# Kernel tuning notes

Hardware: AMD Instinct MI355X
Metric: run time of the kernel (lower is better)

Reference implementation:

```python
import jax, jax.numpy as jnp
import numpy as np
import math
from itertools import combinations

SEQ_LEN = 12
IN_DIM = 1152
D_MODEL = 1152
HEADS = 2
DEPTH = D_MODEL // HEADS
TSS = 3            # temporal_set_size
WAY = 5
SHOT = 5
N_SUPPORT = WAY * SHOT
N_QUERIES = 50
PE_SCALE = 0.1
LN_EPS = 1e-5

# static frame-tuple index table: all C(seq_len, 3) combinations, [T, 3]
TUPLES = np.array(list(combinations(range(SEQ_LEN), TSS)), dtype=np.int32)
T = TUPLES.shape[0]  # 220

def _pe_table():
    pos = np.arange(SEQ_LEN, dtype=np.float64)[:, None]
    div = np.exp(np.arange(0, IN_DIM, 2, dtype=np.float64) * -(math.log(10000.0) / IN_DIM))
    pe = np.zeros((SEQ_LEN, IN_DIM), np.float32)
    pe[:, 0::2] = (np.sin(pos * div) * PE_SCALE).astype(np.float32)
    pe[:, 1::2] = (np.cos(pos * div) * PE_SCALE).astype(np.float32)
    return jnp.asarray(pe)

PE = _pe_table()  # [seq_len, in_dim]

def setup_inputs() -> dict:
    key = jax.random.key(0)
    k0, k1, k2, k3 = jax.random.split(key, 4)
    support_set = jax.random.normal(k0, (N_SUPPORT, SEQ_LEN, IN_DIM), jnp.float32)
    queries = jax.random.normal(k1, (N_QUERIES, SEQ_LEN, IN_DIM), jnp.float32)
    # sorted labels: class c owns support rows [c*SHOT, (c+1)*SHOT)
    support_labels = jnp.repeat(jnp.arange(WAY, dtype=jnp.int32), SHOT)
    k_w = jax.random.normal(k2, (IN_DIM * TSS, D_MODEL), jnp.float32) * 0.02
    k_b = jnp.zeros((D_MODEL,), jnp.float32)
    v_w = jax.random.normal(k3, (IN_DIM * TSS, D_MODEL), jnp.float32) * 0.02
    v_b = jnp.zeros((D_MODEL,), jnp.float32)
    ln_g = jnp.ones((D_MODEL,), jnp.float32)
    ln_b = jnp.zeros((D_MODEL,), jnp.float32)
    return dict(support_set=support_set, queries=queries, support_labels=support_labels,
                k_w=k_w, k_b=k_b, v_w=v_w, v_b=v_b, ln_g=ln_g, ln_b=ln_b)

def _layernorm(x, g, b):
    mu = x.mean(-1, keepdims=True)
    var = ((x - mu) ** 2).mean(-1, keepdims=True)
    return (x - mu) * jax.lax.rsqrt(var + LN_EPS) * g + b

def reference(support_set, queries, support_labels, k_w, k_b, v_w, v_b, ln_g, ln_b):
    nq = queries.shape[0]
    # positional encoding (dropout p=0 -> identity)
    s = support_set + PE
    q = queries + PE
    # temporal tuple gather: [n, T, 3, in_dim] -> [n, T, 3*in_dim]
    s_t = s[:, TUPLES, :].reshape(N_SUPPORT, T, TSS * IN_DIM)
    q_t = q[:, TUPLES, :].reshape(nq, T, TSS * IN_DIM)
    s_ks = _layernorm(s_t @ k_w + k_b, ln_g, ln_b)
    q_ks = _layernorm(q_t @ k_w + k_b, ln_g, ln_b)
    s_vs = s_t @ v_w + v_b
    q_vs = q_t @ v_w + v_b
    # split heads; labels are sorted so class grouping == reshape(way, shot, ...)
    qh = q_ks.reshape(nq, T, HEADS, DEPTH).transpose(0, 2, 1, 3)               # [q,H,T,dh]
    kh = s_ks.reshape(WAY, SHOT, T, HEADS, DEPTH).transpose(0, 1, 3, 2, 4)     # [w,s,H,T,dh]
    vh = s_vs.reshape(WAY, SHOT, T, HEADS, DEPTH).transpose(0, 1, 3, 2, 4)     # [w,s,H,T,dh]
    scores = jnp.einsum('qhtd,wshkd->qwhtsk', qh, kh) / jnp.sqrt(jnp.float32(DEPTH))
    # softmax jointly over (shot, key-tuple) per (query, class, head, query-tuple)
    attn = jax.nn.softmax(scores.reshape(nq, WAY, HEADS, T, SHOT * T), axis=-1)
    attn = attn.reshape(nq, WAY, HEADS, T, SHOT, T)
    # attention output summed over support shots; heads re-concatenated -> prototype
    proto = jnp.einsum('qwhtsk,wshkd->qwthd', attn, vh).reshape(nq, WAY, T, D_MODEL)
    diff = q_vs[:, None, :, :] - proto                                          # [q,w,T,d]
    logits = -(jnp.sum(diff * diff, axis=(-2, -1)) / T)                         # [q,w]
    return logits
```

## Files before the change

### kernel.cpp

```cpp
#include <hip/hip_runtime.h>
#include <math.h>


#define DIM 1152
#define HDIM 576
#define NTUP 220

typedef __attribute__((ext_vector_type(4))) float f32x4;
typedef __attribute__((ext_vector_type(8))) short short8;

__device__ __forceinline__ ushort f2bf(float x) {
  union { float f; unsigned u; } v; v.f = x;
  unsigned r = (v.u + 0x7FFFu + ((v.u >> 16) & 1u)) >> 16;
  return (ushort)r;
}
__device__ __forceinline__ float bf2f(ushort x) {
  union { unsigned u; float f; } v; v.u = ((unsigned)x) << 16;
  return v.f;
}

__global__ __launch_bounds__(256) void init_tables(
    const float* __restrict__ g, const float* __restrict__ bb,
    int* __restrict__ tup, uint* __restrict__ tupP, float* __restrict__ consts)
{
  const int tid = threadIdx.x;
  if (tid < 220) {
    int t = tid, idx = 0;
    for (int a = 0; a < 10; a++)
      for (int b2 = a + 1; b2 < 11; b2++)
        for (int c = b2 + 1; c < 12; c++) {
          if (idx == t) {
            tup[t*3+0]=a; tup[t*3+1]=b2; tup[t*3+2]=c;
            tupP[t] = (uint)a | ((uint)b2 << 8) | ((uint)c << 16);
          }
          idx++;
        }
  }
  __shared__ float rd[6];
  if (tid < 6) rd[tid] = 0.f;
  __syncthreads();
  float s[6] = {0,0,0,0,0,0};
  for (int d = tid; d < DIM; d += 256) {
    float gv = g[d], bv = bb[d];
    int h = (d >= HDIM);
    s[h]     += gv*gv;
    s[2 + h] += gv*bv;
    s[4 + h] += bv*bv;
  }
  for (int i = 0; i < 6; i++) atomicAdd(&rd[i], s[i]);
  __syncthreads();
  if (tid < 6) consts[tid] = rd[tid];
}

__global__ __launch_bounds__(256) void pe_kernel(float* __restrict__ PE)
{
  int idx = blockIdx.x * 256 + threadIdx.x;
  if (idx >= 12 * DIM) return;
  int p = idx / DIM, d = idx - p * DIM;
  int j = d >> 1;
  double div = exp((double)(2 * j) * (-9.210340371976184 / 1152.0));
  double ang = (double)p * div;
  double v = (d & 1) ? cos(ang) : sin(ang);
  PE[idx] = (float)(v * 0.1);
}

__global__ __launch_bounds__(256) void add_pe_bf(
    const float* __restrict__ sup, const float* __restrict__ qry,
    const float* __restrict__ PE, ushort* __restrict__ Fb)
{
  int idx = blockIdx.x * 256 + threadIdx.x;
  if (idx >= 900 * DIM) return;
  int row = idx / DIM, d = idx - row * DIM;
  int p = row % 12;
  float x = (row < 300) ? sup[idx] : qry[idx - 300 * DIM];
  Fb[idx] = f2bf(x + PE[p * DIM + d]);
}

__global__ __launch_bounds__(256) void conv_w(
    const float* __restrict__ kw, const float* __restrict__ vw,
    ushort* __restrict__ Wt)
{
  __shared__ float tileS[32][33];
  const int tid = threadIdx.x;
  const int kt = blockIdx.x * 32;
  const int ng0 = blockIdx.y * 32;
  const int b = ng0 / DIM, d0 = ng0 - b * DIM;
  const float* src = (b < 3) ? (kw + (size_t)b * DIM * DIM)
                             : (vw + (size_t)(b - 3) * DIM * DIM);
  const int r = tid >> 3, cs = (tid & 7) * 4;
  float4 vsrc = *(const float4*)(src + (size_t)(kt + r) * DIM + d0 + cs);
  tileS[r][cs+0] = vsrc.x; tileS[r][cs+1] = vsrc.y;
  tileS[r][cs+2] = vsrc.z; tileS[r][cs+3] = vsrc.w;
  __syncthreads();
  uint u0 = (uint)f2bf(tileS[cs+0][r]) | ((uint)f2bf(tileS[cs+1][r]) << 16);
  uint u1 = (uint)f2bf(tileS[cs+2][r]) | ((uint)f2bf(tileS[cs+3][r]) << 16);
  uint2 o; o.x = u0; o.y = u1;
  *(uint2*)(Wt + (size_t)(ng0 + r) * DIM + kt + cs) = o;
}

__global__ __launch_bounds__(256) void gemm_proj_mfma(
    const ushort* __restrict__ Fb, const ushort* __restrict__ Wt,
    const float* __restrict__ kb, const float* __restrict__ vb,
    float* __restrict__ Ck, float* __restrict__ Cv)
{
  __shared__ __align__(16) ushort As[128][72];
  __shared__ __align__(16) ushort Bs[128][72];
  const int tid = threadIdx.x;
  const int col0 = blockIdx.x * 128;
  const int row0 = blockIdx.y * 128;
  f32x4 acc[4][4] = {};
  const int wv = tid >> 6, lane = tid & 63;
  const int wm = wv >> 1, wn = wv & 1;
  for (int k0 = 0; k0 < DIM; k0 += 64) {
    __syncthreads();
    for (int sidx = tid; sidx < 1024; sidx += 256) {
      int rowa = sidx >> 3, kseg = sidx & 7;
      uint4 va = {0,0,0,0};
      int gm = row0 + rowa;
      if (gm < 900) va = *(const uint4*)(Fb + (size_t)gm * DIM + k0 + kseg * 8);
      *(uint4*)&As[rowa][kseg * 8] = va;
      int gc = col0 + rowa;
      uint4 vb4 = *(const uint4*)(Wt + (size_t)gc * DIM + k0 + kseg * 8);
      *(uint4*)&Bs[rowa][kseg * 8] = vb4;
    }
    __syncthreads();
    #pragma unroll
    for (int ks = 0; ks < 64; ks += 32) {
      short8 a[4], b[4];
      #pragma unroll
      for (int i = 0; i < 4; i++) {
        a[i] = *(const short8*)&As[wm*64 + i*16 + (lane & 15)][ks + (lane >> 4) * 8];
        b[i] = *(const short8*)&Bs[wn*64 + i*16 + (lane & 15)][ks + (lane >> 4) * 8];
      }
      #pragma unroll
      for (int mi = 0; mi < 4; mi++)
        #pragma unroll
        for (int ni = 0; ni < 4; ni++)
          acc[mi][ni] = __builtin_amdgcn_mfma_f32_16x16x32_bf16(a[mi], b[ni], acc[mi][ni], 0, 0, 0);
    }
  }
  const int b = col0 / DIM, d_base = col0 - b * DIM;
  #pragma unroll
  for (int mi = 0; mi < 4; mi++)
    #pragma unroll
    for (int ni = 0; ni < 4; ni++)
      #pragma unroll
      for (int r = 0; r < 4; r++) {
        int m = row0 + wm * 64 + mi * 16 + (lane >> 4) * 4 + r;
        if (m >= 900) continue;
        int n = wn * 64 + ni * 16 + (lane & 15);
        int d = d_base + n;
        float val = acc[mi][ni][r];
        if (b < 3) Ck[((size_t)m * 3 + b)       * DIM + d] = val + kb[d] * (1.f/3.f);
        else       Cv[((size_t)m * 3 + (b - 3)) * DIM + d] = val + vb[d] * (1.f/3.f);
      }
}

__global__ __launch_bounds__(128) void row_stats(
    const float* __restrict__ Ck, const float* __restrict__ g,
    const float* __restrict__ bb, float* __restrict__ m_o,
    float* __restrict__ A_o, float* __restrict__ B_o)
{
  const int r = blockIdx.x, tid = threadIdx.x;
  const float* x = Ck + (size_t)r * DIM;
  float sm = 0, sa0 = 0, sa1 = 0, sb0 = 0, sb1 = 0;
  for (int d = tid; d < DIM; d += 128) {
    float xv = x[d], gv = g[d], bv = bb[d];
    float xg2 = xv * gv * gv, xgb = xv * gv * bv;
    if (d < HDIM) { sa0 += xg2; sb0 += xgb; } else { sa1 += xg2; sb1 += xgb; }
    sm += xv;
  }
  for (int o = 32; o > 0; o >>= 1) {
    sm  += __shfl_down(sm, o);  sa0 += __shfl_down(sa0, o); sa1 += __shfl_down(sa1, o);
    sb0 += __shfl_down(sb0, o); sb1 += __shfl_down(sb1, o);
  }
  __shared__ float red[2][5];
  if ((tid & 63) == 0) {
    int wv = tid >> 6;
    red[wv][0]=sm; red[wv][1]=sa0; red[wv][2]=sa1; red[wv][3]=sb0; red[wv][4]=sb1;
  }
  __syncthreads();
  if (tid == 0) {
    m_o[r]         = (red[0][0] + red[1][0]) * (1.f / 1152.f);
    A_o[r]         =  red[0][1] + red[1][1];
    A_o[2700 + r]  =  red[0][2] + red[1][2];
    B_o[r]         =  red[0][3] + red[1][3];
    B_o[2700 + r]  =  red[0][4] + red[1][4];
  }
}

__global__ __launch_bounds__(256) void self_gram(
    const float* __restrict__ Ck, float* __restrict__ S)
{
  const int u = blockIdx.x, tid = threadIdx.x;
  __shared__ float CS[36][129];
  float acc[2][3] = {{0,0,0},{0,0,0}};
  const int ta = tid / 12, tb = tid - (tid / 12) * 12;
  for (int k0 = 0; k0 < DIM; k0 += 128) {
    __syncthreads();
    for (int idx = tid; idx < 36 * 128; idx += 256) {
      int rr = idx >> 7, kk = idx & 127;
      CS[rr][kk] = Ck[((size_t)u * 36 + rr) * DIM + k0 + kk];
    }
    __syncthreads();
    if (ta < 18) {
      for (int kk = 0; kk < 128; kk++) {
        float va0 = CS[ta*2][kk], va1 = CS[ta*2+1][kk];
        float vb0 = CS[tb*3][kk], vb1 = CS[tb*3+1][kk], vb2 = CS[tb*3+2][kk];
        acc[0][0]+=va0*vb0; acc[0][1]+=va0*vb1; acc[0][2]+=va0*vb2;
        acc[1][0]+=va1*vb0; acc[1][1]+=va1*vb1; acc[1][2]+=va1*vb2;
      }
    }
  }
  if (ta < 18) {
    #pragma unroll
    for (int i = 0; i < 2; i++)
      #pragma unroll
      for (int j = 0; j < 3; j++)
        S[u * 1296 + (ta*2+i) * 36 + tb*3+j] = acc[i][j];
  }
}

__global__ __launch_bounds__(256) void row_ln(
    const float* __restrict__ S, const float* __restrict__ m_i,
    const float* __restrict__ A_i, const float* __restrict__ B_i,
    const int* __restrict__ tup, float4* __restrict__ kst)
{
  const int u = blockIdx.x, tid = threadIdx.x;
  __shared__ float Ss[36][36];
  __shared__ float ms[36], As[2][36], Bs[2][36];
  for (int idx = tid; idx < 1296; idx += 256) (&Ss[0][0])[idx] = S[u * 1296 + idx];
  if (tid < 36) {
    ms[tid]    = m_i[u * 36 + tid];
    As[0][tid] = A_i[u * 36 + tid];  As[1][tid] = A_i[2700 + u * 36 + tid];
    Bs[0][tid] = B_i[u * 36 + tid];  Bs[1][tid] = B_i[2700 + u * 36 + tid];
  }
  __syncthreads();
  if (tid < NTUP) {
    int a0 = tup[tid*3+0]*3+0, a1 = tup[tid*3+1]*3+1, a2 = tup[tid*3+2]*3+2;
    float mu = ms[a0] + ms[a1] + ms[a2];
    float qq = Ss[a0][a0] + Ss[a1][a1] + Ss[a2][a2]
             + 2.f * (Ss[a0][a1] + Ss[a0][a2] + Ss[a1][a2]);
    float var = qq * (1.f / 1152.f) - mu * mu;
    float rr = rsqrtf(var + 1e-5f);
    kst[((size_t)0 * 75 + u) * 220 + tid] =
        make_float4(mu, rr, As[0][a0]+As[0][a1]+As[0][a2], Bs[0][a0]+Bs[0][a1]+Bs[0][a2]);
    kst[((size_t)1 * 75 + u) * 220 + tid] =
        make_float4(mu, rr, As[1][a0]+As[1][a1]+As[1][a2], Bs[1][a0]+Bs[1][a1]+Bs[1][a2]);
  }
}

__global__ __launch_bounds__(256) void conv_ckw(
    const float* __restrict__ Ck, const float* __restrict__ g,
    ushort* __restrict__ Ckw)
{
  size_t i = (size_t)blockIdx.x * 256 + threadIdx.x;
  if (i >= (size_t)2700 * DIM) return;
  int d = (int)(i % DIM);
  Ckw[i] = f2bf(Ck[i] * g[d]);
}

__global__ __launch_bounds__(256) void cross_gram_mfma(
    const ushort* __restrict__ Ckw, ushort* __restrict__ Gb)
{
  __shared__ __align__(16) ushort As[128][72];
  __shared__ __align__(16) ushort Bs[128][72];
  const int tid = threadIdx.x;
  const int col0 = blockIdx.x * 128;
  const int row0 = blockIdx.y * 128;
  const int h = blockIdx.z;
  f32x4 acc[4][4] = {};
  const int wv = tid >> 6, lane = tid & 63;
  const int wm = wv >> 1, wn = wv & 1;
  for (int k0 = 0; k0 < HDIM; k0 += 64) {
    __syncthreads();
    for (int sidx = tid; sidx < 1024; sidx += 256) {
      int rowa = sidx >> 3, kseg = sidx & 7;
      uint4 va = {0,0,0,0};
      int gm = row0 + rowa;
      if (gm < 1800)
        va = *(const uint4*)(Ckw + (size_t)(900 + gm) * DIM + h * HDIM + k0 + kseg * 8);
      *(uint4*)&As[rowa][kseg * 8] = va;
      uint4 vb = {0,0,0,0};
      int gn = col0 + rowa;
      if (gn < 900)
        vb = *(const uint4*)(Ckw + (size_t)gn * DIM + h * HDIM + k0 + kseg * 8);
      *(uint4*)&Bs[rowa][kseg * 8] = vb;
    }
    __syncthreads();
    #pragma unroll
    for (int ks = 0; ks < 64; ks += 32) {
      short8 a[4], b[4];
      #pragma unroll
      for (int i = 0; i < 4; i++) {
        a[i] = *(const short8*)&As[wm*64 + i*16 + (lane & 15)][ks + (lane >> 4) * 8];
        b[i] = *(const short8*)&Bs[wn*64 + i*16 + (lane & 15)][ks + (lane >> 4) * 8];
      }
      #pragma unroll
      for (int mi = 0; mi < 4; mi++)
        #pragma unroll
        for (int ni = 0; ni < 4; ni++)
          acc[mi][ni] = __builtin_amdgcn_mfma_f32_16x16x32_bf16(a[mi], b[ni], acc[mi][ni], 0, 0, 0);
    }
  }
  #pragma unroll
  for (int mi = 0; mi < 4; mi++)
    #pragma unroll
    for (int ni = 0; ni < 4; ni++)
      #pragma unroll
      for (int r = 0; r < 4; r++) {
        int m = row0 + wm * 64 + mi * 16 + (lane >> 4) * 4 + r;
        int n = col0 + wn * 64 + ni * 16 + (lane & 15);
        if (m < 1800 && n < 900)
          Gb[((size_t)h * 1800 + m) * 900 + n] = f2bf(acc[mi][ni][r]);
      }
}

__global__ __launch_bounds__(256) void vt_build(
    const float* __restrict__ Cv, ushort* __restrict__ Vt)
{
  __shared__ ushort T[192][72];
  const int tid = threadIdx.x;
  const int nb = blockIdx.x, z = blockIdx.y;
  const int w = z >> 1, h = z & 1;
  const int n0 = nb * 64;
  for (int idx = tid; idx < 12288; idx += 256) {
    int bin = idx >> 6, nc = idx & 63;
    ushort v = 0;
    if (bin < 180) {
      int s = bin / 36, rem = bin - s * 36, j = rem / 12, p = rem - j * 12;
      v = f2bf(Cv[(size_t)((w*5+s)*36 + p*3 + j) * DIM + h * HDIM + n0 + nc]);
    }
    T[bin][nc] = v;
  }
  __syncthreads();
  for (int u4i = tid; u4i < 1536; u4i += 256) {
    int n = u4i / 24, kc = (u4i - n * 24) * 8;
    ushort tmp[8];
    #pragma unroll
    for (int e = 0; e < 8; e++) tmp[e] = T[kc + e][n];
    *(uint4*)(Vt + ((size_t)z * 576 + n0 + n) * 192 + kc) = *(uint4*)tmp;
  }
}

__global__ __launch_bounds__(256) void attn2(
    const ushort* __restrict__ Gb, const float4* __restrict__ kst,
    const uint* __restrict__ tupP, const float* __restrict__ consts,
    ushort* __restrict__ Mg)
{
  __shared__ __align__(16) ushort GsS[5][36][36];
  __shared__ __align__(16) float4 kstS[5][224];
  __shared__ __align__(16) union UU { ushort Qg[5][16][64]; ushort Ps[2][16][224]; } U;
  __shared__ __align__(16) float4 qstS[112];
  __shared__ uint tupT[224];
  __shared__ float red[4][16];

  const int tid = threadIdx.x;
  const int half = blockIdx.x, w = blockIdx.y;
  const int qu = blockIdx.z >> 1, h = blockIdx.z & 1;
  const float Ggh = consts[h], Gbh = consts[2 + h], Bbh = consts[4 + h];
  const int wv = tid >> 6, lane = tid & 63;
  const int rowg = lane >> 4, col16 = lane & 15;

  for (int idx = tid; idx < 224; idx += 256) tupT[idx] = (idx < 220) ? tupP[idx] : 0u;
  for (int idx = tid; idx < 3240; idx += 256) {
    int s = idx / 648, rem = idx - s * 648, a = rem / 18, bp = rem - a * 18;
    ((uint*)&GsS[s][a][0])[bp] =
      *(const uint*)(Gb + (size_t)(h*1800 + qu*36 + a) * 900 + (w*5+s)*36 + bp*2);
  }
  for (int idx = tid; idx < 1120; idx += 256) {
    int s = idx / 224, k = idx - s * 224;
    float4 v;
    if (k < 220) {
      float4 t4 = kst[((size_t)h*75 + w*5 + s) * 220 + k];
      v = make_float4(t4.x, t4.y, t4.z, (t4.y*(t4.w - t4.x*Gbh) + Bbh) * (1.f/24.f));
    } else v = make_float4(0.f, 0.f, 0.f, -1e30f);
    kstS[s][k] = v;
  }
  for (int idx = tid; idx < 112; idx += 256) {
    int t = half * 112 + idx;
    float4 v = make_float4(0.f, 0.f, 0.f, 0.f);
    if (t < 220) {
      float4 q4 = kst[((size_t)h*75 + 25 + qu) * 220 + t];
      v = make_float4(q4.x, q4.y * (1.f/24.f), q4.z,
                      q4.y * (q4.w - q4.x*Gbh) * (1.f/24.f));
    }
    qstS[idx] = v;
  }
  __syncthreads();

  short8 ebf[4][2];
  #pragma unroll
  for (int i = 0; i < 4; i++) {
    int ntile = wv + 4*i;
    uint tk = tupT[ntile*16 + col16];
    int b0 = (int)(tk & 255u)*3, b1 = (int)((tk>>8)&255u)*3+1, b2 = (int)((tk>>16)&255u)*3+2;
    #pragma unroll
    for (int ks = 0; ks < 2; ks++)
      #pragma unroll
      for (int e = 0; e < 8; e++) {
        int colb = ks*32 + rowg*8 + e;
        ebf[i][ks][e] = (short)((colb==b0 || colb==b1 || colb==b2) ? 0x3F80 : 0);
      }
  }
  short8 lbf[7];
  {
    int bin = wv*16 + col16;
    int j = bin / 12, p = bin - j*12;
    #pragma unroll
    for (int ks = 0; ks < 7; ks++)
      #pragma unroll
      for (int e = 0; e < 8; e++) {
        int k = ks*32 + rowg*8 + e;
        uint tk = tupT[k];
        int f = (j==0) ? (int)(tk & 255u) : (j==1) ? (int)((tk>>8) & 255u)
              : (j==2) ? (int)((tk>>16) & 255u) : 255;
        lbf[ks][e] = (short)((f == p) ? 0x3F80 : 0);
      }
  }

  for (int c = 0; c < 7; c++) {
    const int tbase = (half*7 + c) * 16;
    __syncthreads();
    for (int idx = tid; idx < 5120; idx += 256) {
      int s = idx >> 10, q = (idx >> 6) & 15, b = idx & 63;
      ushort val = 0;
      if (b < 36) {
        uint tq = tupT[tbase + q];
        int a0 = (int)(tq&255u)*3, a1 = (int)((tq>>8)&255u)*3+1, a2 = (int)((tq>>16)&255u)*3+2;
        val = f2bf(bf2f(GsS[s][a0][b]) + bf2f(GsS[s][a1][b]) + bf2f(GsS[s][a2][b]));
      }
      U.Qg[s][q][b] = val;
    }
    __syncthreads();

    float4 q4r[4];
    #pragma unroll
    for (int r = 0; r < 4; r++) q4r[r] = qstS[c*16 + rowg*4 + r];

    f32x4 acc[5][4];
    #pragma unroll
    for (int s = 0; s < 5; s++) {
      short8 af0 = *(const short8*)&U.Qg[s][col16][rowg*8];
      short8 af1 = *(const short8*)&U.Qg[s][col16][32 + rowg*8];
      #pragma unroll
      for (int i = 0; i < 4; i++) {
        int ntile = wv + 4*i;
        if (ntile < 14) {
          f32x4 a4 = {0.f,0.f,0.f,0.f};
          a4 = __builtin_amdgcn_mfma_f32_16x16x32_bf16(af0, ebf[i][0], a4, 0, 0, 0);
          a4 = __builtin_amdgcn_mfma_f32_16x16x32_bf16(af1, ebf[i][1], a4, 0, 0, 0);
          float4 k4 = kstS[s][ntile*16 + col16];
          #pragma unroll
          for (int r = 0; r < 4; r++) {
            float X = a4[r] - k4.x * q4r[r].z - q4r[r].x * (k4.z - k4.x * Ggh);
            a4[r] = q4r[r].y * k4.y * X + q4r[r].w + k4.w;
          }
          acc[s][i] = a4;
        }
      }
    }

    float mxr[4] = {-1e30f,-1e30f,-1e30f,-1e30f};
    #pragma unroll
    for (int s = 0; s < 5; s++)
      #pragma unroll
      for (int i = 0; i < 4; i++)
        if (wv + 4*i < 14) {
          #pragma unroll
          for (int r = 0; r < 4; r++) mxr[r] = fmaxf(mxr[r], acc[s][i][r]);
        }
    #pragma unroll
    for (int o = 8; o > 0; o >>= 1) {
      #pragma unroll
      for (int r = 0; r < 4; r++) mxr[r] = fmaxf(mxr[r], __shfl_xor(mxr[r], o));
    }
    if (col16 == 0) {
      #pragma unroll
      for (int r = 0; r < 4; r++) red[wv][rowg*4 + r] = mxr[r];
    }
    __syncthreads();
    float mxg[4];
    #pragma unroll
    for (int r = 0; r < 4; r++) {
      int row = rowg*4 + r;
      mxg[r] = fmaxf(fmaxf(red[0][row], red[1][row]), fmaxf(red[2][row], red[3][row]));
    }
    __syncthreads();
    float smr[4] = {0.f,0.f,0.f,0.f};
    #pragma unroll
    for (int s = 0; s < 5; s++)
      #pragma unroll
      for (int i = 0; i < 4; i++)
        if (wv + 4*i < 14) {
          #pragma unroll
          for (int r = 0; r < 4; r++) {
            float p = __expf(acc[s][i][r] - mxg[r]);
            acc[s][i][r] = p;
            smr[r] += p;
          }
        }
    #pragma unroll
    for (int o = 8; o > 0; o >>= 1) {
      #pragma unroll
      for (int r = 0; r < 4; r++) smr[r] += __shfl_xor(smr[r], o);
    }
    if (col16 == 0) {
      #pragma unroll
      for (int r = 0; r < 4; r++) red[wv][rowg*4 + r] = smr[r];
    }
    __syncthreads();
    float inv[4];
    #pragma unroll
    for (int r = 0; r < 4; r++) {
      int row = rowg*4 + r;
      inv[r] = 1.0f / (red[0][row] + red[1][row] + red[2][row] + red[3][row]);
    }

    #pragma unroll
    for (int s = 0; s < 5; s++) {
      #pragma unroll
      for (int i = 0; i < 4; i++) {
        int ntile = wv + 4*i;
        if (ntile < 14) {
          #pragma unroll
          for (int r = 0; r < 4; r++)
            U.Ps[s & 1][rowg*4 + r][ntile*16 + col16] = f2bf(acc[s][i][r]);
        }
      }
      __syncthreads();
      if (wv < 3) {
        f32x4 macc = {0.f,0.f,0.f,0.f};
        #pragma unroll
        for (int ks = 0; ks < 7; ks++) {
          short8 pa = *(const short8*)&U.Ps[s & 1][col16][ks*32 + rowg*8];
          macc = __builtin_amdgcn_mfma_f32_16x16x32_bf16(pa, lbf[ks], macc, 0, 0, 0);
        }
        int bin = wv*16 + col16;
        if (bin < 36) {
          #pragma unroll
          for (int r = 0; r < 4; r++) {
            int t = tbase + rowg*4 + r;
            if (t < 220)
              Mg[(((size_t)(h*50 + qu)*5 + w)*220 + t)*192 + s*36 + bin] =
                  f2bf(macc[r] * inv[r]);
          }
        }
      }
    }
  }
}

__global__ __launch_bounds__(256) void pv_kernel(
    const ushort* __restrict__ Mg, const ushort* __restrict__ Vt,
    const float* __restrict__ Cv, const uint* __restrict__ tupP,
    float* __restrict__ out)
{
  __shared__ __align__(16) ushort As[128][72];
  __shared__ __align__(16) ushort Bs[128][72];
  __shared__ uint tupS[224];
  __shared__ float redL[4][2];
  const int tid = threadIdx.x;
  const int nb = blockIdx.x, mb = blockIdx.y, z = blockIdx.z;
  const int w = z >> 1, h = z & 1;
  const int m0 = mb * 128, n0 = nb * 128;
  const int wv = tid >> 6, lane = tid & 63;
  const int wm = wv >> 1, wn = wv & 1;
  const int rowg = lane >> 4, col16 = lane & 15;
  for (int idx = tid; idx < 224; idx += 256) tupS[idx] = (idx < 220) ? tupP[idx] : 0u;

  f32x4 acc[4][4] = {};
  for (int k0 = 0; k0 < 192; k0 += 64) {
    __syncthreads();
    for (int sidx = tid; sidx < 1024; sidx += 256) {
      int row = sidx >> 3, seg = sidx & 7;
      int gm = m0 + row;
      uint4 va = {0,0,0,0};
      if (gm < 11000) {
        int qu = gm / 220, t = gm - qu * 220;
        va = *(const uint4*)(Mg + (((size_t)(h*50 + qu)*5 + w)*220 + t)*192 + k0 + seg*8);
      }
      *(uint4*)&As[row][seg*8] = va;
      int gn = n0 + row;
      uint4 vb = {0,0,0,0};
      if (gn < 576)
        vb = *(const uint4*)(Vt + ((size_t)z*576 + gn)*192 + k0 + seg*8);
      *(uint4*)&Bs[row][seg*8] = vb;
    }
    __syncthreads();
    #pragma unroll
    for (int ks = 0; ks < 2; ks++) {
      short8 a[4], b[4];
      #pragma unroll
      for (int i = 0; i < 4; i++) {
        a[i] = *(const short8*)&As[wm*64 + i*16 + col16][ks*32 + rowg*8];
        b[i] = *(const short8*)&Bs[wn*64 + i*16 + col16][ks*32 + rowg*8];
      }
      #pragma unroll
      for (int mi = 0; mi < 4; mi++)
        #pragma unroll
        for (int ni = 0; ni < 4; ni++)
          acc[mi][ni] = __builtin_amdgcn_mfma_f32_16x16x32_bf16(a[mi], b[ni], acc[mi][ni], 0, 0, 0);
    }
  }
  const int quA = m0 / 220;
  const int mB = (quA + 1) * 220;
  float sq0 = 0.f, sq1 = 0.f;
  #pragma unroll
  for (int mi = 0; mi < 4; mi++) {
    #pragma unroll
    for (int r = 0; r < 4; r++) {
      int m = m0 + wm*64 + mi*16 + rowg*4 + r;
      if (m >= 11000) continue;
      int qu = (m >= mB) ? quA + 1 : quA;
      int t = m - qu * 220;
      uint tq = tupS[t];
      int f0 = (int)(tq & 255u), f1 = (int)((tq>>8) & 255u), f2v = (int)((tq>>16) & 255u);
      const float* c0 = Cv + (size_t)((25+qu)*36 + f0*3 + 0) * DIM + h * HDIM;
      const float* c1 = Cv + (size_t)((25+qu)*36 + f1*3 + 1) * DIM + h * HDIM;
      const float* c2 = Cv + (size_t)((25+qu)*36 + f2v*3 + 2) * DIM + h * HDIM;
      #pragma unroll
      for (int ni = 0; ni < 4; ni++) {
        int n = n0 + wn*64 + ni*16 + col16;
        if (n < 576) {
          float qv = c0[n] + c1[n] + c2[n];
          float d = qv - acc[mi][ni][r];
          float s2 = d * d;
          if (qu == quA) sq0 += s2; else sq1 += s2;
        }
      }
    }
  }
  #pragma unroll
  for (int o = 32; o > 0; o >>= 1) {
    sq0 += __shfl_down(sq0, o);
    sq1 += __shfl_down(sq1, o);
  }
  if (lane == 0) { redL[wv][0] = sq0; redL[wv][1] = sq1; }
  __syncthreads();
  if (tid == 0) {
    float t0 = redL[0][0] + redL[1][0] + redL[2][0] + redL[3][0];
    float t1 = redL[0][1] + redL[1][1] + redL[2][1] + redL[3][1];
    atomicAdd(&out[quA*5 + w], -t0 * (1.0f/220.0f));
    if (quA + 1 < 50 && t1 != 0.f)
      atomicAdd(&out[(quA+1)*5 + w], -t1 * (1.0f/220.0f));
  }
}

extern "C" void kernel_launch(void* const* d_in, const int* in_sizes, int n_in,
                              void* d_out, int out_size, void* d_ws, size_t ws_size,
                              hipStream_t stream) {
  const float* support = (const float*)d_in[0];
  const float* queries = (const float*)d_in[1];
  const float* kw = (const float*)d_in[3];
  const float* kb = (const float*)d_in[4];
  const float* vw = (const float*)d_in[5];
  const float* vb = (const float*)d_in[6];
  const float* g  = (const float*)d_in[7];
  const float* bb = (const float*)d_in[8];
  float* out = (float*)d_out;

  float* ws = (float*)d_ws;
  size_t off = 0;
  auto alloc = [&](size_t n) { float* p = ws + off; off += (n + 63) & ~(size_t)63; return p; };
  float* PE   = alloc(12 * DIM);
  float* r1   = alloc(10560000);
  ushort* Fb  = (ushort*)r1;
  ushort* Ckw = (ushort*)r1;
  ushort* Mg  = (ushort*)r1;
  float* r2   = alloc(3981312);
  ushort* Wt  = (ushort*)r2;
  ushort* Gb  = (ushort*)r2;
  float* Ck   = alloc((size_t)2700 * DIM);
  float* Cv   = alloc((size_t)2700 * DIM);
  float* m_arr = alloc(2700);
  float* A_arr = alloc(2 * 2700);
  float* B_arr = alloc(2 * 2700);
  float* S     = alloc(75 * 1296);
  float4* kst  = (float4*)alloc(2 * 75 * 220 * 4);
  float* consts = alloc(64);
  int* tup   = (int*)alloc(660);
  uint* tupP = (uint*)alloc(256);
  float* VtF = alloc(552960);
  ushort* Vt = (ushort*)VtF;

  hipMemsetAsync(d_out, 0, (size_t)out_size * sizeof(float), stream);

  init_tables<<<1, 256, 0, stream>>>(g, bb, tup, tupP, consts);
  pe_kernel<<<(12 * DIM + 255) / 256, 256, 0, stream>>>(PE);
  add_pe_bf<<<(900 * DIM + 255) / 256, 256, 0, stream>>>(support, queries, PE, Fb);
  conv_w<<<dim3(36, 216), 256, 0, stream>>>(kw, vw, Wt);
  gemm_proj_mfma<<<dim3(54, 8), 256, 0, stream>>>(Fb, Wt, kb, vb, Ck, Cv);
  row_stats<<<2700, 128, 0, stream>>>(Ck, g, bb, m_arr, A_arr, B_arr);
  self_gram<<<75, 256, 0, stream>>>(Ck, S);
  row_ln<<<75, 256, 0, stream>>>(S, m_arr, A_arr, B_arr, tup, kst);
  conv_ckw<<<(int)(((size_t)2700 * DIM + 255) / 256), 256, 0, stream>>>(Ck, g, Ckw);
  cross_gram_mfma<<<dim3(8, 15, 2), 256, 0, stream>>>(Ckw, Gb);
  vt_build<<<dim3(9, 10), 256, 0, stream>>>(Cv, Vt);
  hipMemsetAsync(Mg, 0, (size_t)500 * 220 * 192 * 2, stream);
  attn2<<<dim3(2, 5, 100), 256, 0, stream>>>(Gb, kst, tupP, consts, Mg);
  pv_kernel<<<dim3(5, 86, 10), 256, 0, stream>>>(Mg, Vt, Cv, tupP, out);
}
```

Before: 930.5 us.

## Fuse prep kernels, split self-gram over K, replace Mg memset with pad zeroing

```diff
diff --git a/kernel.cpp b/kernel.cpp
--- a/kernel.cpp
+++ b/kernel.cpp
@@ -19,11 +19,27 @@
   return v.f;
 }
 
-__global__ __launch_bounds__(256) void init_tables(
+__global__ __launch_bounds__(256) void prep(
+    const float* __restrict__ sup, const float* __restrict__ qry,
     const float* __restrict__ g, const float* __restrict__ bb,
-    int* __restrict__ tup, uint* __restrict__ tupP, float* __restrict__ consts)
+    ushort* __restrict__ Fb, int* __restrict__ tup, uint* __restrict__ tupP,
+    float* __restrict__ consts)
 {
   const int tid = threadIdx.x;
+  const int b = blockIdx.x;
+  if (b < 900) {
+    const int p = b % 12;
+    const float* src = (b < 300) ? (sup + (size_t)b * DIM)
+                                 : (qry + (size_t)(b - 300) * DIM);
+    for (int d = tid; d < DIM; d += 256) {
+      int j = d >> 1;
+      float div = expf((float)(2 * j) * (-9.210340371976184f / 1152.0f));
+      float ang = (float)p * div;
+      float pe = ((d & 1) ? cosf(ang) : sinf(ang)) * 0.1f;
+      Fb[(size_t)b * DIM + d] = f2bf(src[d] + pe);
+    }
+    return;
+  }
   if (tid < 220) {
     int t = tid, idx = 0;
     for (int a = 0; a < 10; a++)
@@ -36,9 +52,6 @@
           idx++;
         }
   }
-  __shared__ float rd[6];
-  if (tid < 6) rd[tid] = 0.f;
-  __syncthreads();
   float s[6] = {0,0,0,0,0,0};
   for (int d = tid; d < DIM; d += 256) {
     float gv = g[d], bv = bb[d];
@@ -47,33 +60,17 @@
     s[2 + h] += gv*bv;
     s[4 + h] += bv*bv;
   }
-  for (int i = 0; i < 6; i++) atomicAdd(&rd[i], s[i]);
+  __shared__ float red[4][6];
+  #pragma unroll
+  for (int i = 0; i < 6; i++)
+    #pragma unroll
+    for (int o = 32; o > 0; o >>= 1) s[i] += __shfl_down(s[i], o);
+  if ((tid & 63) == 0) {
+    #pragma unroll
+    for (int i = 0; i < 6; i++) red[tid >> 6][i] = s[i];
+  }
   __syncthreads();
-  if (tid < 6) consts[tid] = rd[tid];
-}
-
-__global__ __launch_bounds__(256) void pe_kernel(float* __restrict__ PE)
-{
-  int idx = blockIdx.x * 256 + threadIdx.x;
-  if (idx >= 12 * DIM) return;
-  int p = idx / DIM, d = idx - p * DIM;
-  int j = d >> 1;
-  double div = exp((double)(2 * j) * (-9.210340371976184 / 1152.0));
-  double ang = (double)p * div;
-  double v = (d & 1) ? cos(ang) : sin(ang);
-  PE[idx] = (float)(v * 0.1);
-}
-
-__global__ __launch_bounds__(256) void add_pe_bf(
-    const float* __restrict__ sup, const float* __restrict__ qry,
-    const float* __restrict__ PE, ushort* __restrict__ Fb)
-{
-  int idx = blockIdx.x * 256 + threadIdx.x;
-  if (idx >= 900 * DIM) return;
-  int row = idx / DIM, d = idx - row * DIM;
-  int p = row % 12;
-  float x = (row < 300) ? sup[idx] : qry[idx - 300 * DIM];
-  Fb[idx] = f2bf(x + PE[p * DIM + d]);
+  if (tid < 6) consts[tid] = red[0][tid] + red[1][tid] + red[2][tid] + red[3][tid];
 }
 
 __global__ __launch_bounds__(256) void conv_w(
@@ -192,11 +189,12 @@
 __global__ __launch_bounds__(256) void self_gram(
     const float* __restrict__ Ck, float* __restrict__ S)
 {
-  const int u = blockIdx.x, tid = threadIdx.x;
+  const int u = blockIdx.x, part = blockIdx.y, tid = threadIdx.x;
   __shared__ float CS[36][129];
   float acc[2][3] = {{0,0,0},{0,0,0}};
   const int ta = tid / 12, tb = tid - (tid / 12) * 12;
-  for (int k0 = 0; k0 < DIM; k0 += 128) {
+  const int kbase = part * 384;
+  for (int k0 = kbase; k0 < kbase + 384; k0 += 128) {
     __syncthreads();
     for (int idx = tid; idx < 36 * 128; idx += 256) {
       int rr = idx >> 7, kk = idx & 127;
@@ -217,7 +215,7 @@
     for (int i = 0; i < 2; i++)
       #pragma unroll
       for (int j = 0; j < 3; j++)
-        S[u * 1296 + (ta*2+i) * 36 + tb*3+j] = acc[i][j];
+        S[((size_t)part * 75 + u) * 1296 + (ta*2+i) * 36 + tb*3+j] = acc[i][j];
   }
 }
 
@@ -229,7 +227,10 @@
   const int u = blockIdx.x, tid = threadIdx.x;
   __shared__ float Ss[36][36];
   __shared__ float ms[36], As[2][36], Bs[2][36];
-  for (int idx = tid; idx < 1296; idx += 256) (&Ss[0][0])[idx] = S[u * 1296 + idx];
+  for (int idx = tid; idx < 1296; idx += 256)
+    (&Ss[0][0])[idx] = S[(size_t)u * 1296 + idx]
+                     + S[(size_t)(75 + u) * 1296 + idx]
+                     + S[(size_t)(150 + u) * 1296 + idx];
   if (tid < 36) {
     ms[tid]    = m_i[u * 36 + tid];
     As[0][tid] = A_i[u * 36 + tid];  As[1][tid] = A_i[2700 + u * 36 + tid];
@@ -548,6 +549,12 @@
         }
       }
     }
+    if (tid < 96) {
+      int q = tid / 6, cp = tid - (tid / 6) * 6;
+      int t = tbase + q;
+      if (t < 220)
+        *(uint*)&Mg[(((size_t)(h*50 + qu)*5 + w)*220 + t)*192 + 180 + cp*2] = 0u;
+    }
   }
 }
 
@@ -663,7 +670,6 @@
   float* ws = (float*)d_ws;
   size_t off = 0;
   auto alloc = [&](size_t n) { float* p = ws + off; off += (n + 63) & ~(size_t)63; return p; };
-  float* PE   = alloc(12 * DIM);
   float* r1   = alloc(10560000);
   ushort* Fb  = (ushort*)r1;
   ushort* Ckw = (ushort*)r1;
@@ -676,7 +682,7 @@
   float* m_arr = alloc(2700);
   float* A_arr = alloc(2 * 2700);
   float* B_arr = alloc(2 * 2700);
-  float* S     = alloc(75 * 1296);
+  float* S     = alloc(3 * 75 * 1296);
   float4* kst  = (float4*)alloc(2 * 75 * 220 * 4);
   float* consts = alloc(64);
   int* tup   = (int*)alloc(660);
@@ -686,18 +692,15 @@
 
   hipMemsetAsync(d_out, 0, (size_t)out_size * sizeof(float), stream);
 
-  init_tables<<<1, 256, 0, stream>>>(g, bb, tup, tupP, consts);
-  pe_kernel<<<(12 * DIM + 255) / 256, 256, 0, stream>>>(PE);
-  add_pe_bf<<<(900 * DIM + 255) / 256, 256, 0, stream>>>(support, queries, PE, Fb);
+  prep<<<901, 256, 0, stream>>>(support, queries, g, bb, Fb, tup, tupP, consts);
   conv_w<<<dim3(36, 216), 256, 0, stream>>>(kw, vw, Wt);
   gemm_proj_mfma<<<dim3(54, 8), 256, 0, stream>>>(Fb, Wt, kb, vb, Ck, Cv);
   row_stats<<<2700, 128, 0, stream>>>(Ck, g, bb, m_arr, A_arr, B_arr);
-  self_gram<<<75, 256, 0, stream>>>(Ck, S);
+  self_gram<<<dim3(75, 3), 256, 0, stream>>>(Ck, S);
   row_ln<<<75, 256, 0, stream>>>(S, m_arr, A_arr, B_arr, tup, kst);
   conv_ckw<<<(int)(((size_t)2700 * DIM + 255) / 256), 256, 0, stream>>>(Ck, g, Ckw);
   cross_gram_mfma<<<dim3(8, 15, 2), 256, 0, stream>>>(Ckw, Gb);
   vt_build<<<dim3(9, 10), 256, 0, stream>>>(Cv, Vt);
-  hipMemsetAsync(Mg, 0, (size_t)500 * 220 * 192 * 2, stream);
   attn2<<<dim3(2, 5, 100), 256, 0, stream>>>(Gb, kst, tupP, consts, Mg);
   pv_kernel<<<dim3(5, 86, 10), 256, 0, stream>>>(Mg, Vt, Cv, tupP, out);
 }
```

New measurement: 866.7 us. 1.07x faster.
